# Kernel optimization log

Hardware: AMD Instinct MI355X
Metric: run time of the kernel (lower is better)

Reference implementation:

```python
import jax, jax.numpy as jnp
import numpy as np

B, T, C = 4, 2048, 2048
H, HD = 16, 128  # n_heads, head_dim; C == H*HD


def _rope_rotate(x, cos, sin):
    """x: [b,t,h,d]; cos/sin: [t, d//2]. Complex multiply on interleaved pairs,
    matching torch view_as_complex on reshape(..., -1, 2)."""
    xr = x[..., 0::2]  # real parts  [b,t,h,d/2]
    xi = x[..., 1::2]  # imag parts
    c = cos[None, :, None, :]
    s = sin[None, :, None, :]
    or_ = xr * c - xi * s
    oi_ = xr * s + xi * c
    # interleave back: [..., d/2, 2] -> [..., d]
    return jnp.stack([or_, oi_], axis=-1).reshape(x.shape)


def setup_inputs() -> dict:
    key = jax.random.key(0)
    ks = jax.random.split(key, 6)
    x = jax.random.normal(ks[0], (B, T, C), dtype=jnp.float32)
    # causal boolean mask: True = attend
    attn_mask = jnp.tril(jnp.ones((T, T), dtype=bool))
    # standard RoPE frequencies (theta=10000)
    inv_freq = 1.0 / (10000.0 ** (np.arange(0, HD, 2, dtype=np.float32) / HD))
    ang = np.arange(T, dtype=np.float32)[:, None] * inv_freq[None, :]  # [T, HD/2]
    rope_cos = jnp.asarray(np.cos(ang))
    rope_sin = jnp.asarray(np.sin(ang))
    sc = 1.0 / np.sqrt(C)
    Wq = jax.random.normal(ks[1], (C, C), dtype=jnp.float32) * sc
    Wk = jax.random.normal(ks[2], (C, C), dtype=jnp.float32) * sc
    Wv = jax.random.normal(ks[3], (C, C), dtype=jnp.float32) * sc
    Wp = jax.random.normal(ks[4], (C, C), dtype=jnp.float32) * sc
    return {"x": x, "attn_mask": attn_mask, "rope_cos": rope_cos,
            "rope_sin": rope_sin, "Wq": Wq, "Wk": Wk, "Wv": Wv, "Wp": Wp}


def reference(x, attn_mask, rope_cos, rope_sin, Wq, Wk, Wv, Wp):
    b, t, c = x.shape
    # QKV projections (nn.Linear: y = x @ W.T), reshape to heads
    q = jnp.einsum('btc,dc->btd', x, Wq).reshape(b, t, H, HD)
    k = jnp.einsum('btc,dc->btd', x, Wk).reshape(b, t, H, HD)
    v = jnp.einsum('btc,dc->btd', x, Wv).reshape(b, t, H, HD)
    # RoPE on q, k
    q = _rope_rotate(q, rope_cos[:t], rope_sin[:t])
    k = _rope_rotate(k, rope_cos[:t], rope_sin[:t])
    # SDPA with boolean mask, scale 1/sqrt(head_dim)
    scores = jnp.einsum('bqhd,bkhd->bhqk', q, k) / jnp.sqrt(jnp.asarray(HD, x.dtype))
    neg = jnp.finfo(scores.dtype).min
    scores = jnp.where(attn_mask[None, None, :t, :t], scores, neg)
    attn = jax.nn.softmax(scores, axis=-1)
    out = jnp.einsum('bhqk,bkhd->bqhd', attn, v).reshape(b, t, H * HD)
    return jnp.einsum('btd,cd->btc', out, Wp)
```

## Files before the change

kernel.cpp:

```cpp
#include <hip/hip_runtime.h>

#define B_    4
#define T_    2048
#define C_    2048
#define H_    16
#define HD_   128
#define LDQK  4096

typedef __attribute__((ext_vector_type(8))) short short8v;
typedef __attribute__((ext_vector_type(4))) float float4v;
typedef __attribute__((ext_vector_type(16))) float float16v;

typedef const __attribute__((address_space(1))) void* gld_src_t;
typedef __attribute__((address_space(3))) void* gld_dst_t;
#define GLDS16(g, l) __builtin_amdgcn_global_load_lds((gld_src_t)(g), (gld_dst_t)(l), 16, 0, 0)

__device__ __forceinline__ unsigned short f2bf(float f) {
  unsigned int u = __float_as_uint(f);
  u += 0x7fffu + ((u >> 16) & 1u);
  return (unsigned short)(u >> 16);
}
__device__ __forceinline__ float bf2f(unsigned short s) {
  return __uint_as_float(((unsigned int)s) << 16);
}
__device__ __forceinline__ unsigned int cvtpk_bf16(float lo, float hi) {
  unsigned int r;
  asm("v_cvt_pk_bf16_f32 %0, %1, %2" : "=v"(r) : "v"(lo), "v"(hi));
  return r;
}

__global__ void cvt_kernel(const float* __restrict__ src, unsigned short* __restrict__ dst, int n4) {
  int i = blockIdx.x * blockDim.x + threadIdx.x;
  if (i >= n4) return;
  float4 v = reinterpret_cast<const float4*>(src)[i];
  ushort4 o;
  o.x = f2bf(v.x); o.y = f2bf(v.y); o.z = f2bf(v.z); o.w = f2bf(v.w);
  reinterpret_cast<ushort4*>(dst)[i] = o;
}


#define ISSUE_HALF(MAT, HA, KT, CBUF)                                             \
  { const unsigned short* gp_ = (MAT) ? Bm : A;                                   \
    const size_t gb_ = (MAT) ? bbase : abase;                                     \
    _Pragma("unroll")                                                             \
    for (int i_ = 0; i_ < 2; ++i_) {                                              \
      int fo_ = (i_ * 512 + tid) * 16;                              \
      int rl_ = fo_ >> 7;                                            \
      int row_ = (HA) * 128 + rl_;                                                \
      int g_ = (fo_ >> 4) & 7;                                                    \
      int ce_ = ((g_ ^ (rl_ & 7)) << 3);              \
      GLDS16(gp_ + gb_ + (size_t)row_ * K + (KT) * 64 + ce_,                      \
             lds + (CBUF) * 65536 + (MAT) * 32768 + (HA) * 16384 + fo_);          \
    } }

#define RD_A(dst, MI, KK, CBUF)                                                   \
  { int row_ = wm * 128 + (MI) * 16 + lr;                                         \
    dst = *reinterpret_cast<const short8v*>(                                      \
        lds + (CBUF) * 65536 + row_ * 128 + (((KK) * 64 + lg * 16) ^ ((row_ & 7) << 4))); }

#define RD_B(dst, NI, KK, CBUF)                                                   \
  { int row_ = wn * 64 + (NI) * 16 + lr;                                          \
    dst = *reinterpret_cast<const short8v*>(                                      \
        lds + (CBUF) * 65536 + 32768 + row_ * 128 + (((KK) * 64 + lg * 16) ^ ((row_ & 7) << 4))); }

#define MFMA_BLOCK(MBASE, BV)                                                     \
  { __builtin_amdgcn_s_setprio(1);                                                \
    _Pragma("unroll")                                                             \
    for (int ni_ = 0; ni_ < 4; ++ni_) {                                           \
      acc[(MBASE)+0][ni_] = __builtin_amdgcn_mfma_f32_16x16x32_bf16(a0, BV[ni_], acc[(MBASE)+0][ni_], 0,0,0); \
      acc[(MBASE)+1][ni_] = __builtin_amdgcn_mfma_f32_16x16x32_bf16(a1, BV[ni_], acc[(MBASE)+1][ni_], 0,0,0); \
      acc[(MBASE)+2][ni_] = __builtin_amdgcn_mfma_f32_16x16x32_bf16(a2, BV[ni_], acc[(MBASE)+2][ni_], 0,0,0); \
      acc[(MBASE)+3][ni_] = __builtin_amdgcn_mfma_f32_16x16x32_bf16(a3, BV[ni_], acc[(MBASE)+3][ni_], 0,0,0); \
    }                                                                             \
    __builtin_amdgcn_s_setprio(0); }

#define FENCE asm volatile("" ::: "memory")

template<int MODE>
__global__ __launch_bounds__(512, 2)
void gemm256(const unsigned short* __restrict__ A, const unsigned short* __restrict__ Bm,
             void* __restrict__ Cout, int K, int NB, int ldc)
{
  extern __shared__ char lds[];
  const int tid = threadIdx.x;
  const int l = tid & 63, w = tid >> 6;
  const int lr = l & 15, lg = l >> 4;
  const int wm = w >> 2, wn = w & 3;

  const int nwg = (int)gridDim.x;
  const int orig = (int)blockIdx.x;
  const int qq = nwg >> 3, rr = nwg & 7;
  const int xcd = orig & 7, idx = orig >> 3;
  const int wg = (xcd < rr ? xcd * (qq + 1) : rr * (qq + 1) + (xcd - rr) * qq) + idx;
  const int bm = wg / NB, bn = wg % NB;

  const size_t abase = (size_t)bm * 256 * (size_t)K;
  const size_t bbase = (size_t)bn * 256 * (size_t)K;

  float4v acc[8][4];
  const float4v fz = {0.f, 0.f, 0.f, 0.f};
#pragma unroll
  for (int i = 0; i < 8; ++i)
#pragma unroll
    for (int j = 0; j < 4; ++j) acc[i][j] = fz;

  const int nk = K >> 6;

  ISSUE_HALF(1, 0, 0, 0)
  ISSUE_HALF(1, 1, 0, 0)
  ISSUE_HALF(0, 0, 0, 0)
  ISSUE_HALF(0, 1, 0, 0)
  asm volatile("s_waitcnt vmcnt(0)" ::: "memory");
  __builtin_amdgcn_s_barrier();
  FENCE;

  short8v a0, a1, a2, a3;
  short8v bv0[4], bv1[4];

  for (int t = 0; t < nk; ++t) {
    const int c = t & 1;

    if (t + 1 < nk) {
      ISSUE_HALF(1, 0, t + 1, c ^ 1)
      ISSUE_HALF(1, 1, t + 1, c ^ 1)
      ISSUE_HALF(0, 0, t + 1, c ^ 1)
      ISSUE_HALF(0, 1, t + 1, c ^ 1)
    }
    FENCE;

    RD_A(a0, 0, 0, c) RD_A(a1, 1, 0, c) RD_A(a2, 2, 0, c) RD_A(a3, 3, 0, c)
    RD_B(bv0[0], 0, 0, c) RD_B(bv0[1], 1, 0, c) RD_B(bv0[2], 2, 0, c) RD_B(bv0[3], 3, 0, c)
    MFMA_BLOCK(0, bv0)
    RD_A(a0, 4, 0, c) RD_A(a1, 5, 0, c) RD_A(a2, 6, 0, c) RD_A(a3, 7, 0, c)
    MFMA_BLOCK(4, bv0)
    RD_A(a0, 0, 1, c) RD_A(a1, 1, 1, c) RD_A(a2, 2, 1, c) RD_A(a3, 3, 1, c)
    RD_B(bv1[0], 0, 1, c) RD_B(bv1[1], 1, 1, c) RD_B(bv1[2], 2, 1, c) RD_B(bv1[3], 3, 1, c)
    MFMA_BLOCK(0, bv1)
    RD_A(a0, 4, 1, c) RD_A(a1, 5, 1, c) RD_A(a2, 6, 1, c) RD_A(a3, 7, 1, c)
    MFMA_BLOCK(4, bv1)

    asm volatile("s_waitcnt vmcnt(0)" ::: "memory");
    __builtin_amdgcn_s_barrier();
    FENCE;
  }

  const int row0 = bm * 256 + wm * 128;
  const int col0 = bn * 256 + wn * 64;
  if (MODE == 2) {
    unsigned short* vtp = (unsigned short*)Cout;
#pragma unroll
    for (int mi = 0; mi < 8; ++mi)
#pragma unroll
      for (int ni = 0; ni < 4; ++ni) {
        int col = col0 + ni * 16 + lr;
        int hh = col >> 7, dd = col & 127;
        int row = row0 + mi * 16 + lg * 4;
        int bb = row >> 11, t0 = row & 2047;
        ushort4 o4;
        o4.x = f2bf(acc[mi][ni][0]); o4.y = f2bf(acc[mi][ni][1]);
        o4.z = f2bf(acc[mi][ni][2]); o4.w = f2bf(acc[mi][ni][3]);
        *reinterpret_cast<ushort4*>(vtp + (((size_t)(bb * 16 + hh)) << 18) + (((size_t)dd) << 11) + t0) = o4;
      }
  } else {
#pragma unroll
    for (int mi = 0; mi < 8; ++mi)
#pragma unroll
      for (int ni = 0; ni < 4; ++ni)
#pragma unroll
        for (int r2 = 0; r2 < 4; ++r2) {
          int row = row0 + mi * 16 + lg * 4 + r2;
          int col = col0 + ni * 16 + lr;
          float v = acc[mi][ni][r2];
          if (MODE == 1)
            ((unsigned short*)Cout)[(size_t)row * ldc + col] = f2bf(v);
          else
            ((float*)Cout)[(size_t)row * ldc + col] = v;
        }
  }
}

__global__ void rope_kernel(unsigned short* __restrict__ qk,
                            const float* __restrict__ cosb, const float* __restrict__ sinb)
{
  int i = blockIdx.x * blockDim.x + threadIdx.x;
  int seg = i & 15;
  int h   = (i >> 4) & (H_ - 1);
  int bt  = i >> 8;
  if (bt >= B_ * T_) return;
  int t = bt & (T_ - 1);

  float4 cv = *reinterpret_cast<const float4*>(cosb + t * 64 + seg * 4);
  float4 sv = *reinterpret_cast<const float4*>(sinb + t * 64 + seg * 4);
  float cc[4] = {cv.x, cv.y, cv.z, cv.w};
  float ss[4] = {sv.x, sv.y, sv.z, sv.w};

  size_t base = (size_t)bt * LDQK + h * HD_ + seg * 8;
#pragma unroll
  for (int qkx = 0; qkx < 2; ++qkx) {
    unsigned short* p = qk + base + qkx * 2048;
    uint4 u = *reinterpret_cast<uint4*>(p);
    unsigned int* uu = reinterpret_cast<unsigned int*>(&u);
#pragma unroll
    for (int j = 0; j < 4; ++j) {
      float xr = bf2f((unsigned short)(uu[j] & 0xffffu));
      float xi = bf2f((unsigned short)(uu[j] >> 16));
      float orr = xr * cc[j] - xi * ss[j];
      float oii = xr * ss[j] + xi * cc[j];
      uu[j] = (unsigned int)f2bf(orr) | ((unsigned int)f2bf(oii) << 16);
    }
    *reinterpret_cast<uint4*>(p) = u;
  }
}

__global__ __launch_bounds__(256, 2)
void attn_kernel(const unsigned short* __restrict__ qk,
                 const unsigned short* __restrict__ vt,
                 unsigned short* __restrict__ out)
{
  __shared__ unsigned short Kl[2][64 * 128];
  __shared__ unsigned short Vl[2][128 * 64];

  const int wg = (int)blockIdx.x;
  const int bh = ((wg >> 6) << 3) | (wg & 7);
  const int bx = (wg >> 3) & 7;
  const int b = bh >> 4, h = bh & 15;
  const int tid = threadIdx.x, w = tid >> 6, l = tid & 63;
  const int q32 = l & 31, hi = l >> 5;
  const size_t rowbase = (size_t)b * T_;
  const unsigned short* kbase = qk + rowbase * LDQK + 2048 + h * HD_;
  const unsigned short* vbase = vt + (size_t)bh * (HD_ * (size_t)T_);
  const float SC = 0.12754089f;
  const float16v z16 = {0.f,0.f,0.f,0.f,0.f,0.f,0.f,0.f,0.f,0.f,0.f,0.f,0.f,0.f,0.f,0.f};

#define STAGE(kv0_, bi_)                                                          \
  {                                                                               \
    _Pragma("unroll")                                                             \
    for (int i_ = 0; i_ < 4; ++i_) {                                              \
      int fo = (i_ * 256 + tid) * 16;                                             \
      int row = fo >> 8;                                                          \
      int cb = (fo & 255) ^ ((row & 15) << 4);                                    \
      GLDS16(kbase + (size_t)((kv0_) + row) * LDQK + (cb >> 1), (char*)Kl[bi_] + fo); \
    }                                                                             \
    _Pragma("unroll")                                                             \
    for (int i_ = 0; i_ < 4; ++i_) {                                              \
      int fo = (i_ * 256 + tid) * 16;                                             \
      int r6 = (fo >> 8) & 63;                                                    \
      int s_ = (fo >> 7) & 1;                                                     \
      int dd = r6 | ((s_ ^ ((r6 >> 3) & 1)) << 6);                                \
      int k16 = ((fo >> 4) & 7) ^ (dd & 7);                                       \
      GLDS16(vbase + (size_t)dd * T_ + (kv0_) + k16 * 8, (char*)Vl[bi_] + fo);    \
    }                                                                             \
  }

  for (int sel = 0; sel < 2; ++sel) {
    const int qt = sel ? bx : (15 - bx);
    const int q0w = qt * 128 + w * 32;
    const int qg = q0w + q32;

    short8v qf[8];
#pragma unroll
    for (int kf = 0; kf < 8; ++kf) {
      short8v t = *reinterpret_cast<const short8v*>(
          qk + (rowbase + q0w + q32) * (size_t)LDQK + h * HD_ + kf * 16 + hi * 8);
      short8v r;
#pragma unroll
      for (int e = 0; e < 8; ++e) r[e] = (short)f2bf(bf2f((unsigned short)t[e]) * SC);
      qf[kf] = r;
    }

    float16v o[4];
#pragma unroll
    for (int db = 0; db < 4; ++db) o[db] = z16;
    float m_run = -1e30f, lsum = 0.f;

    const int nkv = 2 * (qt + 1);

    STAGE(0, 0);
    __syncthreads();

    for (int tile = 0; tile < nkv; ++tile) {
      const int kv0 = tile * 64;
      const int bi = tile & 1;
      if (tile + 1 < nkv) STAGE((tile + 1) * 64, bi ^ 1);

      if (kv0 <= q0w + 31) {
        float16v stv[2];
        stv[0] = z16; stv[1] = z16;
        __builtin_amdgcn_s_setprio(1);
#pragma unroll
        for (int kb = 0; kb < 2; ++kb) {
          int key = kb * 32 + q32;
          int swz = (key & 15) << 4;
          int rbase = key * 256;
#pragma unroll
          for (int kf = 0; kf < 8; ++kf) {
            short8v ak = *reinterpret_cast<const short8v*>(
                (char*)Kl[bi] + rbase + ((kf * 32 + hi * 16) ^ swz));
            stv[kb] = __builtin_amdgcn_mfma_f32_32x32x16_bf16(ak, qf[kf], stv[kb], 0, 0, 0);
          }
        }
        __builtin_amdgcn_s_setprio(0);
        if (kv0 + 63 > q0w) {
#pragma unroll
          for (int kb = 0; kb < 2; ++kb)
#pragma unroll
            for (int r = 0; r < 16; ++r) {
              int key = kv0 + kb * 32 + (r & 3) + 8 * ((r >> 2) & 3) + 4 * hi;
              if (key > qg) stv[kb][r] = -1e30f;
            }
        }
        float t16[16];
#pragma unroll
        for (int r = 0; r < 16; ++r) t16[r] = fmaxf(stv[0][r], stv[1][r]);
#pragma unroll
        for (int s = 8; s >= 1; s >>= 1)
#pragma unroll
          for (int r = 0; r < s; ++r) t16[r] = fmaxf(t16[r], t16[r + s]);
        float pm = fmaxf(t16[0], __shfl_xor(t16[0], 32));

        if (!__all(pm <= m_run + 8.0f)) {
          float mn = fmaxf(m_run, pm);
          float fac = exp2f(m_run - mn);
          lsum *= fac;
          m_run = mn;
#pragma unroll
          for (int r = 0; r < 16; ++r) {
            int src = (r & 3) + 8 * ((r >> 2) & 3) + 4 * hi;
            float fr = __shfl(fac, src);
#pragma unroll
            for (int db = 0; db < 4; ++db) o[db][r] *= fr;
          }
        }
        {
          float s16[16];
#pragma unroll
          for (int r = 0; r < 16; ++r) {
            float p0 = exp2f(stv[0][r] - m_run);
            float p1 = exp2f(stv[1][r] - m_run);
            stv[0][r] = p0; stv[1][r] = p1;
            s16[r] = p0 + p1;
          }
#pragma unroll
          for (int s = 8; s >= 1; s >>= 1)
#pragma unroll
            for (int r = 0; r < s; ++r) s16[r] += s16[r + s];
          lsum += s16[0] + __shfl_xor(s16[0], 32);
        }
        unsigned int pw0[8], pw1[8], xw0[8], xw1[8];
#pragma unroll
        for (int j = 0; j < 8; ++j) {
          pw0[j] = cvtpk_bf16(stv[0][2 * j], stv[0][2 * j + 1]);
          pw1[j] = cvtpk_bf16(stv[1][2 * j], stv[1][2 * j + 1]);
        }
#pragma unroll
        for (int j = 0; j < 8; ++j) {
          xw0[j] = __shfl_xor(pw0[j], 32);
          xw1[j] = __shfl_xor(pw1[j], 32);
        }
        union UW { unsigned int u[4]; short8v v; };
        short8v pb[4];
        {
          UW a0, a1, c0, c1;
          a0.u[0] = hi ? xw0[2] : pw0[0];  a0.u[1] = hi ? xw0[3] : pw0[1];
          a0.u[2] = hi ? pw0[2] : xw0[0];  a0.u[3] = hi ? pw0[3] : xw0[1];
          a1.u[0] = hi ? xw0[6] : pw0[4];  a1.u[1] = hi ? xw0[7] : pw0[5];
          a1.u[2] = hi ? pw0[6] : xw0[4];  a1.u[3] = hi ? pw0[7] : xw0[5];
          c0.u[0] = hi ? xw1[2] : pw1[0];  c0.u[1] = hi ? xw1[3] : pw1[1];
          c0.u[2] = hi ? pw1[2] : xw1[0];  c0.u[3] = hi ? pw1[3] : xw1[1];
          c1.u[0] = hi ? xw1[6] : pw1[4];  c1.u[1] = hi ? xw1[7] : pw1[5];
          c1.u[2] = hi ? pw1[6] : xw1[4];  c1.u[3] = hi ? pw1[7] : xw1[5];
          pb[0] = a0.v; pb[1] = a1.v; pb[2] = c0.v; pb[3] = c1.v;
        }
        __builtin_amdgcn_s_setprio(1);
#pragma unroll
        for (int db = 0; db < 4; ++db) {
          int dd = db * 32 + q32;
          int rb2 = (dd & 63) * 256 + ((((dd >> 6) ^ ((dd >> 3) & 1)) & 1) << 7);
          int swz = (dd & 7) << 4;
#pragma unroll
          for (int kb16 = 0; kb16 < 4; ++kb16) {
            short8v bv = *reinterpret_cast<const short8v*>(
                (char*)Vl[bi] + rb2 + ((kb16 * 32 + hi * 16) ^ swz));
            o[db] = __builtin_amdgcn_mfma_f32_32x32x16_bf16(pb[kb16], bv, o[db], 0, 0, 0);
          }
        }
        __builtin_amdgcn_s_setprio(0);
      }
      __syncthreads();
    }

    float linv = 1.0f / lsum;
#pragma unroll
    for (int r = 0; r < 16; ++r) {
      int src = (r & 3) + 8 * ((r >> 2) & 3) + 4 * hi;
      float lr_ = __shfl(linv, src);
      size_t rowoff = (rowbase + q0w + src) * (size_t)C_ + h * HD_ + q32;
#pragma unroll
      for (int db = 0; db < 4; ++db)
        out[rowoff + db * 32] = f2bf(o[db][r] * lr_);
    }
  }
#undef STAGE
}

extern "C" void kernel_launch(void* const* d_in, const int* in_sizes, int n_in,
                              void* d_out, int out_size, void* d_ws, size_t ws_size,
                              hipStream_t stream) {
  (void)in_sizes; (void)n_in; (void)out_size; (void)ws_size;
  const float* x  = (const float*)d_in[0];
  const float* rc = (const float*)d_in[2];
  const float* rs = (const float*)d_in[3];
  const float* Wq = (const float*)d_in[4];
  const float* Wk = (const float*)d_in[5];
  const float* Wv = (const float*)d_in[6];
  const float* Wp = (const float*)d_in[7];
  float* outp = (float*)d_out;

  unsigned short* ws    = (unsigned short*)d_ws;
  unsigned short* x_bf  = ws;
  unsigned short* wqkv  = x_bf + 16777216;
  unsigned short* wp_bf = wqkv + 12582912;
  unsigned short* qkbuf = wp_bf + 4194304;
  unsigned short* vtbuf = qkbuf + 33554432;
  unsigned short* ao    = x_bf;

  hipFuncSetAttribute((const void*)gemm256<0>, hipFuncAttributeMaxDynamicSharedMemorySize, 131072);
  hipFuncSetAttribute((const void*)gemm256<1>, hipFuncAttributeMaxDynamicSharedMemorySize, 131072);
  hipFuncSetAttribute((const void*)gemm256<2>, hipFuncAttributeMaxDynamicSharedMemorySize, 131072);

  cvt_kernel<<<16384, 256, 0, stream>>>(x,  x_bf, 4194304);
  cvt_kernel<<<4096,  256, 0, stream>>>(Wq, wqkv,            1048576);
  cvt_kernel<<<4096,  256, 0, stream>>>(Wk, wqkv + 4194304,  1048576);
  cvt_kernel<<<4096,  256, 0, stream>>>(Wv, wqkv + 8388608,  1048576);
  cvt_kernel<<<4096,  256, 0, stream>>>(Wp, wp_bf,           1048576);

  gemm256<1><<<dim3(512), 512, 131072, stream>>>(x_bf, wqkv, qkbuf, 2048, 16, 4096);
  gemm256<2><<<dim3(256), 512, 131072, stream>>>(x_bf, wqkv + 8388608, vtbuf, 2048, 8, 0);

  rope_kernel<<<8192, 256, 0, stream>>>(qkbuf, rc, rs);

  attn_kernel<<<dim3(512), 256, 0, stream>>>(qkbuf, vtbuf, ao);

  gemm256<0><<<dim3(256), 512, 131072, stream>>>(ao, wp_bf, outp, 2048, 8, 2048);
}
```

Measured before the change: 425.6 us.

## Restructure GEMM main loop into barrier-phased MFMA stages and fuse conversion kernels

The GEMM inner loop is split into four phases, each separated by workgroup barriers with setprio around the MFMA blocks. The next-tile global-to-LDS loads are interleaved between phases rather than issued all at once at the top. This aims to stagger waves so that LDS reads, global loads and MFMAs from the two co-resident workgroups overlap better. Separately, the five fp32-to-bf16 conversion launches are merged into one kernel, relying on wp_bf being contiguous after wqkv. The extra barriers add synchronization cost and may stall waves if the phases are poorly balanced.

```diff
diff --git a/kernel.cpp b/kernel.cpp
--- a/kernel.cpp
+++ b/kernel.cpp
@@ -29,13 +29,27 @@
   return r;
 }
 
-__global__ void cvt_kernel(const float* __restrict__ src, unsigned short* __restrict__ dst, int n4) {
+__global__ void cvt5_kernel(const float* __restrict__ x,
+                            const float* __restrict__ wq, const float* __restrict__ wk,
+                            const float* __restrict__ wv, const float* __restrict__ wp,
+                            unsigned short* __restrict__ xbf, unsigned short* __restrict__ wdst) {
   int i = blockIdx.x * blockDim.x + threadIdx.x;
-  if (i >= n4) return;
-  float4 v = reinterpret_cast<const float4*>(src)[i];
+  const float4* s;
+  ushort4* d;
+  if (i < 4194304) {
+    s = reinterpret_cast<const float4*>(x) + i;
+    d = reinterpret_cast<ushort4*>(xbf) + i;
+  } else {
+    int j = i - 4194304;
+    int w = j >> 20;
+    const float* wsrc = (w == 0) ? wq : (w == 1) ? wk : (w == 2) ? wv : wp;
+    s = reinterpret_cast<const float4*>(wsrc) + (j & 1048575);
+    d = reinterpret_cast<ushort4*>(wdst) + j;
+  }
+  float4 v = *s;
   ushort4 o;
   o.x = f2bf(v.x); o.y = f2bf(v.y); o.z = f2bf(v.z); o.w = f2bf(v.w);
-  reinterpret_cast<ushort4*>(dst)[i] = o;
+  *d = o;
 }
 
 
@@ -63,18 +77,24 @@
     dst = *reinterpret_cast<const short8v*>(                                      \
         lds + (CBUF) * 65536 + 32768 + row_ * 128 + (((KK) * 64 + lg * 16) ^ ((row_ & 7) << 4))); }
 
-#define MFMA_BLOCK(MBASE, BV)                                                     \
-  { __builtin_amdgcn_s_setprio(1);                                                \
+#define MFMA16(MB, A0_, A1_, A2_, A3_, BV)                                        \
     _Pragma("unroll")                                                             \
     for (int ni_ = 0; ni_ < 4; ++ni_) {                                           \
-      acc[(MBASE)+0][ni_] = __builtin_amdgcn_mfma_f32_16x16x32_bf16(a0, BV[ni_], acc[(MBASE)+0][ni_], 0,0,0); \
-      acc[(MBASE)+1][ni_] = __builtin_amdgcn_mfma_f32_16x16x32_bf16(a1, BV[ni_], acc[(MBASE)+1][ni_], 0,0,0); \
-      acc[(MBASE)+2][ni_] = __builtin_amdgcn_mfma_f32_16x16x32_bf16(a2, BV[ni_], acc[(MBASE)+2][ni_], 0,0,0); \
-      acc[(MBASE)+3][ni_] = __builtin_amdgcn_mfma_f32_16x16x32_bf16(a3, BV[ni_], acc[(MBASE)+3][ni_], 0,0,0); \
-    }                                                                             \
-    __builtin_amdgcn_s_setprio(0); }
-
-#define FENCE asm volatile("" ::: "memory")
+      acc[(MB)+0][ni_] = __builtin_amdgcn_mfma_f32_16x16x32_bf16(A0_, BV[ni_], acc[(MB)+0][ni_], 0,0,0); \
+      acc[(MB)+1][ni_] = __builtin_amdgcn_mfma_f32_16x16x32_bf16(A1_, BV[ni_], acc[(MB)+1][ni_], 0,0,0); \
+      acc[(MB)+2][ni_] = __builtin_amdgcn_mfma_f32_16x16x32_bf16(A2_, BV[ni_], acc[(MB)+2][ni_], 0,0,0); \
+      acc[(MB)+3][ni_] = __builtin_amdgcn_mfma_f32_16x16x32_bf16(A3_, BV[ni_], acc[(MB)+3][ni_], 0,0,0); \
+    }
+
+#define PHASE_PRE                                                                 \
+    __builtin_amdgcn_s_barrier();                                                 \
+    asm volatile("s_waitcnt lgkmcnt(0)" ::: "memory");                            \
+    __builtin_amdgcn_sched_barrier(0);                                            \
+    __builtin_amdgcn_s_setprio(1);
+
+#define PHASE_POST                                                                \
+    __builtin_amdgcn_s_setprio(0);                                                \
+    __builtin_amdgcn_s_barrier();
 
 template<int MODE>
 __global__ __launch_bounds__(512, 2)
@@ -112,36 +132,40 @@
   ISSUE_HALF(0, 1, 0, 0)
   asm volatile("s_waitcnt vmcnt(0)" ::: "memory");
   __builtin_amdgcn_s_barrier();
-  FENCE;
-
-  short8v a0, a1, a2, a3;
-  short8v bv0[4], bv1[4];
+
+  short8v aA0, aA1, aA2, aA3;
+  short8v aB0, aB1, aB2, aB3;
+  short8v bA[4], bB[4];
 
   for (int t = 0; t < nk; ++t) {
     const int c = t & 1;
-
-    if (t + 1 < nk) {
-      ISSUE_HALF(1, 0, t + 1, c ^ 1)
-      ISSUE_HALF(1, 1, t + 1, c ^ 1)
-      ISSUE_HALF(0, 0, t + 1, c ^ 1)
-      ISSUE_HALF(0, 1, t + 1, c ^ 1)
-    }
-    FENCE;
-
-    RD_A(a0, 0, 0, c) RD_A(a1, 1, 0, c) RD_A(a2, 2, 0, c) RD_A(a3, 3, 0, c)
-    RD_B(bv0[0], 0, 0, c) RD_B(bv0[1], 1, 0, c) RD_B(bv0[2], 2, 0, c) RD_B(bv0[3], 3, 0, c)
-    MFMA_BLOCK(0, bv0)
-    RD_A(a0, 4, 0, c) RD_A(a1, 5, 0, c) RD_A(a2, 6, 0, c) RD_A(a3, 7, 0, c)
-    MFMA_BLOCK(4, bv0)
-    RD_A(a0, 0, 1, c) RD_A(a1, 1, 1, c) RD_A(a2, 2, 1, c) RD_A(a3, 3, 1, c)
-    RD_B(bv1[0], 0, 1, c) RD_B(bv1[1], 1, 1, c) RD_B(bv1[2], 2, 1, c) RD_B(bv1[3], 3, 1, c)
-    MFMA_BLOCK(0, bv1)
-    RD_A(a0, 4, 1, c) RD_A(a1, 5, 1, c) RD_A(a2, 6, 1, c) RD_A(a3, 7, 1, c)
-    MFMA_BLOCK(4, bv1)
-
+    const bool pf = (t + 1 < nk);
+
+    RD_A(aA0, 0, 0, c) RD_A(aA1, 1, 0, c) RD_A(aA2, 2, 0, c) RD_A(aA3, 3, 0, c)
+    RD_B(bA[0], 0, 0, c) RD_B(bA[1], 1, 0, c) RD_B(bA[2], 2, 0, c) RD_B(bA[3], 3, 0, c)
+    if (pf) { ISSUE_HALF(1, 0, t + 1, c ^ 1) ISSUE_HALF(1, 1, t + 1, c ^ 1) }
+    PHASE_PRE
+    MFMA16(0, aA0, aA1, aA2, aA3, bA)
+    PHASE_POST
+
+    RD_A(aB0, 4, 0, c) RD_A(aB1, 5, 0, c) RD_A(aB2, 6, 0, c) RD_A(aB3, 7, 0, c)
+    if (pf) { ISSUE_HALF(0, 0, t + 1, c ^ 1) ISSUE_HALF(0, 1, t + 1, c ^ 1) }
+    PHASE_PRE
+    MFMA16(4, aB0, aB1, aB2, aB3, bA)
+    PHASE_POST
+
+    RD_A(aA0, 0, 1, c) RD_A(aA1, 1, 1, c) RD_A(aA2, 2, 1, c) RD_A(aA3, 3, 1, c)
+    RD_B(bB[0], 0, 1, c) RD_B(bB[1], 1, 1, c) RD_B(bB[2], 2, 1, c) RD_B(bB[3], 3, 1, c)
+    PHASE_PRE
+    MFMA16(0, aA0, aA1, aA2, aA3, bB)
+    PHASE_POST
+
+    RD_A(aB0, 4, 1, c) RD_A(aB1, 5, 1, c) RD_A(aB2, 6, 1, c) RD_A(aB3, 7, 1, c)
+    PHASE_PRE
+    MFMA16(4, aB0, aB1, aB2, aB3, bB)
+    __builtin_amdgcn_s_setprio(0);
     asm volatile("s_waitcnt vmcnt(0)" ::: "memory");
     __builtin_amdgcn_s_barrier();
-    FENCE;
   }
 
   const int row0 = bm * 256 + wm * 128;
@@ -428,11 +452,7 @@
   hipFuncSetAttribute((const void*)gemm256<1>, hipFuncAttributeMaxDynamicSharedMemorySize, 131072);
   hipFuncSetAttribute((const void*)gemm256<2>, hipFuncAttributeMaxDynamicSharedMemorySize, 131072);
 
-  cvt_kernel<<<16384, 256, 0, stream>>>(x,  x_bf, 4194304);
-  cvt_kernel<<<4096,  256, 0, stream>>>(Wq, wqkv,            1048576);
-  cvt_kernel<<<4096,  256, 0, stream>>>(Wk, wqkv + 4194304,  1048576);
-  cvt_kernel<<<4096,  256, 0, stream>>>(Wv, wqkv + 8388608,  1048576);
-  cvt_kernel<<<4096,  256, 0, stream>>>(Wp, wp_bf,           1048576);
+  cvt5_kernel<<<32768, 256, 0, stream>>>(x, Wq, Wk, Wv, Wp, x_bf, wqkv);
 
   gemm256<1><<<dim3(512), 512, 131072, stream>>>(x_bf, wqkv, qkbuf, 2048, 16, 4096);
   gemm256<2><<<dim3(256), 512, 131072, stream>>>(x_bf, wqkv + 8388608, vtbuf, 2048, 8, 0);
```

After: 422.6 us. Within noise of the previous version (-0.7%).

## Fuse QKV GEMMs with RoPE epilogue and merge conversion kernels

Applied to the files above, without the earlier changes.

Merges the five fp32-to-bf16 conversion launches into one kernel. Merges the QK and V projection GEMMs into a single 768-block launch whose epilogue applies RoPE via lane shuffles before storing QK, or writes V transposed. This removes the separate RoPE pass over the QK buffer and several launches, at the cost of scalar cos/sin loads and per-element stores in the GEMM epilogue. wp_bf is assumed contiguous after wqkv, so Wp conversion writes into it.

```diff
diff --git a/kernel.cpp b/kernel.cpp
--- a/kernel.cpp
+++ b/kernel.cpp
@@ -29,13 +29,27 @@
   return r;
 }
 
-__global__ void cvt_kernel(const float* __restrict__ src, unsigned short* __restrict__ dst, int n4) {
+__global__ void cvt5_kernel(const float* __restrict__ x,
+                            const float* __restrict__ wq, const float* __restrict__ wk,
+                            const float* __restrict__ wv, const float* __restrict__ wp,
+                            unsigned short* __restrict__ xbf, unsigned short* __restrict__ wdst) {
   int i = blockIdx.x * blockDim.x + threadIdx.x;
-  if (i >= n4) return;
-  float4 v = reinterpret_cast<const float4*>(src)[i];
+  const float4* s;
+  ushort4* d;
+  if (i < 4194304) {
+    s = reinterpret_cast<const float4*>(x) + i;
+    d = reinterpret_cast<ushort4*>(xbf) + i;
+  } else {
+    int j = i - 4194304;
+    int w = j >> 20;
+    const float* wsrc = (w == 0) ? wq : (w == 1) ? wk : (w == 2) ? wv : wp;
+    s = reinterpret_cast<const float4*>(wsrc) + (j & 1048575);
+    d = reinterpret_cast<ushort4*>(wdst) + j;
+  }
+  float4 v = *s;
   ushort4 o;
   o.x = f2bf(v.x); o.y = f2bf(v.y); o.z = f2bf(v.z); o.w = f2bf(v.w);
-  reinterpret_cast<ushort4*>(dst)[i] = o;
+  *d = o;
 }
 
 
@@ -79,7 +93,9 @@
 template<int MODE>
 __global__ __launch_bounds__(512, 2)
 void gemm256(const unsigned short* __restrict__ A, const unsigned short* __restrict__ Bm,
-             void* __restrict__ Cout, int K, int NB, int ldc)
+             void* __restrict__ Cout, unsigned short* __restrict__ vtp,
+             int K, int NB, int ldc,
+             const float* __restrict__ rc, const float* __restrict__ rs)
 {
   extern __shared__ char lds[];
   const int tid = threadIdx.x;
@@ -146,14 +162,13 @@
 
   const int row0 = bm * 256 + wm * 128;
   const int col0 = bn * 256 + wn * 64;
-  if (MODE == 2) {
-    unsigned short* vtp = (unsigned short*)Cout;
+  if (MODE == 3 && bn >= 16) {
 #pragma unroll
     for (int mi = 0; mi < 8; ++mi)
 #pragma unroll
       for (int ni = 0; ni < 4; ++ni) {
-        int col = col0 + ni * 16 + lr;
-        int hh = col >> 7, dd = col & 127;
+        int vcol = col0 - 4096 + ni * 16 + lr;
+        int hh = vcol >> 7, dd = vcol & 127;
         int row = row0 + mi * 16 + lg * 4;
         int bb = row >> 11, t0 = row & 2047;
         ushort4 o4;
@@ -161,6 +176,26 @@
         o4.z = f2bf(acc[mi][ni][2]); o4.w = f2bf(acc[mi][ni][3]);
         *reinterpret_cast<ushort4*>(vtp + (((size_t)(bb * 16 + hh)) << 18) + (((size_t)dd) << 11) + t0) = o4;
       }
+  } else if (MODE == 3) {
+    const float sgn = (lr & 1) ? 1.0f : -1.0f;
+#pragma unroll
+    for (int mi = 0; mi < 8; ++mi)
+#pragma unroll
+      for (int ni = 0; ni < 4; ++ni) {
+        int col = col0 + ni * 16 + lr;
+        int ii = (col & 127) >> 1;
+#pragma unroll
+        for (int r2 = 0; r2 < 4; ++r2) {
+          int row = row0 + mi * 16 + lg * 4 + r2;
+          int tt = row & 2047;
+          float v = acc[mi][ni][r2];
+          float vp = __shfl_xor(v, 1);
+          float cs = rc[tt * 64 + ii];
+          float sn = rs[tt * 64 + ii];
+          float o = v * cs + sgn * vp * sn;
+          ((unsigned short*)Cout)[(size_t)row * ldc + col] = f2bf(o);
+        }
+      }
   } else {
 #pragma unroll
     for (int mi = 0; mi < 8; ++mi)
@@ -170,45 +205,8 @@
         for (int r2 = 0; r2 < 4; ++r2) {
           int row = row0 + mi * 16 + lg * 4 + r2;
           int col = col0 + ni * 16 + lr;
-          float v = acc[mi][ni][r2];
-          if (MODE == 1)
-            ((unsigned short*)Cout)[(size_t)row * ldc + col] = f2bf(v);
-          else
-            ((float*)Cout)[(size_t)row * ldc + col] = v;
-        }
-  }
-}
-
-__global__ void rope_kernel(unsigned short* __restrict__ qk,
-                            const float* __restrict__ cosb, const float* __restrict__ sinb)
-{
-  int i = blockIdx.x * blockDim.x + threadIdx.x;
-  int seg = i & 15;
-  int h   = (i >> 4) & (H_ - 1);
-  int bt  = i >> 8;
-  if (bt >= B_ * T_) return;
-  int t = bt & (T_ - 1);
-
-  float4 cv = *reinterpret_cast<const float4*>(cosb + t * 64 + seg * 4);
-  float4 sv = *reinterpret_cast<const float4*>(sinb + t * 64 + seg * 4);
-  float cc[4] = {cv.x, cv.y, cv.z, cv.w};
-  float ss[4] = {sv.x, sv.y, sv.z, sv.w};
-
-  size_t base = (size_t)bt * LDQK + h * HD_ + seg * 8;
-#pragma unroll
-  for (int qkx = 0; qkx < 2; ++qkx) {
-    unsigned short* p = qk + base + qkx * 2048;
-    uint4 u = *reinterpret_cast<uint4*>(p);
-    unsigned int* uu = reinterpret_cast<unsigned int*>(&u);
-#pragma unroll
-    for (int j = 0; j < 4; ++j) {
-      float xr = bf2f((unsigned short)(uu[j] & 0xffffu));
-      float xi = bf2f((unsigned short)(uu[j] >> 16));
-      float orr = xr * cc[j] - xi * ss[j];
-      float oii = xr * ss[j] + xi * cc[j];
-      uu[j] = (unsigned int)f2bf(orr) | ((unsigned int)f2bf(oii) << 16);
-    }
-    *reinterpret_cast<uint4*>(p) = u;
+          ((float*)Cout)[(size_t)row * ldc + col] = acc[mi][ni][r2];
+        }
   }
 }
 
@@ -425,21 +423,13 @@
   unsigned short* ao    = x_bf;
 
   hipFuncSetAttribute((const void*)gemm256<0>, hipFuncAttributeMaxDynamicSharedMemorySize, 131072);
-  hipFuncSetAttribute((const void*)gemm256<1>, hipFuncAttributeMaxDynamicSharedMemorySize, 131072);
-  hipFuncSetAttribute((const void*)gemm256<2>, hipFuncAttributeMaxDynamicSharedMemorySize, 131072);
-
-  cvt_kernel<<<16384, 256, 0, stream>>>(x,  x_bf, 4194304);
-  cvt_kernel<<<4096,  256, 0, stream>>>(Wq, wqkv,            1048576);
-  cvt_kernel<<<4096,  256, 0, stream>>>(Wk, wqkv + 4194304,  1048576);
-  cvt_kernel<<<4096,  256, 0, stream>>>(Wv, wqkv + 8388608,  1048576);
-  cvt_kernel<<<4096,  256, 0, stream>>>(Wp, wp_bf,           1048576);
-
-  gemm256<1><<<dim3(512), 512, 131072, stream>>>(x_bf, wqkv, qkbuf, 2048, 16, 4096);
-  gemm256<2><<<dim3(256), 512, 131072, stream>>>(x_bf, wqkv + 8388608, vtbuf, 2048, 8, 0);
-
-  rope_kernel<<<8192, 256, 0, stream>>>(qkbuf, rc, rs);
+  hipFuncSetAttribute((const void*)gemm256<3>, hipFuncAttributeMaxDynamicSharedMemorySize, 131072);
+
+  cvt5_kernel<<<32768, 256, 0, stream>>>(x, Wq, Wk, Wv, Wp, x_bf, wqkv);
+
+  gemm256<3><<<dim3(768), 512, 131072, stream>>>(x_bf, wqkv, qkbuf, vtbuf, 2048, 24, 4096, rc, rs);
 
   attn_kernel<<<dim3(512), 256, 0, stream>>>(qkbuf, vtbuf, ao);
 
-  gemm256<0><<<dim3(256), 512, 131072, stream>>>(ao, wp_bf, outp, 2048, 8, 2048);
-}
+  gemm256<0><<<dim3(256), 512, 131072, stream>>>(ao, wp_bf, outp, nullptr, 2048, 8, 2048, nullptr, nullptr);
+}
```

Result: faster. 414.7 us (-2.6%).
